# Kernel tuning notes

Measured on AMD Instinct MI355X. Metric: run time of the kernel, lower is better.

The kernel has to match this reference:

```python
import jax, jax.numpy as jnp
import numpy as np

# ---- constants from init_kwargs ----
RES = 128                       # config.grid.resolution (base_resolution, n_levels=1)
LOG2_T = 22
TABLE_SIZE = 1 << LOG2_T        # hashmap entries
N_G = 4                         # features per level, gaussian grid
N_V = 8                         # features per level, vmf grid
BB_MIN = jnp.array([-10.0, -10.0, -10.0], dtype=jnp.float32)
BB_MAX = jnp.array([10.0, 10.0, 10.0], dtype=jnp.float32)
N_PTS = 1048576

_P2 = np.uint32(2654435761)
_P3 = np.uint32(805459861)
# 8 trilinear corner offsets [8,3]
_CORNERS = jnp.array([[i, j, k] for i in (0, 1) for j in (0, 1) for k in (0, 1)], dtype=jnp.int32)


def hashgrid_lookup(table, pos):
    """tcnn-style HashGrid (1 level, trilinear). pos: [N,3] in [0,1] domain."""
    x = pos * RES                     # scale to grid coords
    x0 = jnp.floor(x)
    w = x - x0                        # [N,3] trilinear weights
    corners = x0.astype(jnp.int32)[:, None, :] + _CORNERS[None]   # [N,8,3]
    cu = corners.astype(jnp.uint32)
    h = (cu[..., 0] ^ (cu[..., 1] * _P2) ^ (cu[..., 2] * _P3)) & jnp.uint32(TABLE_SIZE - 1)
    feat = table[h.astype(jnp.int32)]                              # [N,8,F] gather
    wts = jnp.prod(jnp.where(_CORNERS[None].astype(bool), w[:, None, :], 1.0 - w[:, None, :]), axis=-1)  # [N,8]
    return jnp.einsum('nc,ncf->nf', wts, feat)                     # [N,F]


def sample_vpls(pos, gauss_table, vmf_table):
    """Accumulate encodings over the 27-neighbor stencil (accumulate_gaussians=True)."""
    block = 1.0 / RES
    npos = (pos - BB_MIN) / (BB_MAX - BB_MIN)      # normalized [N,3]
    total_g = jnp.zeros((pos.shape[0], N_G), dtype=jnp.float32)
    total_v = jnp.zeros((pos.shape[0], N_V), dtype=jnp.float32)
    for dx in (-1, 0, 1):
        for dy in (-1, 0, 1):
            for dz in (-1, 0, 1):
                off = jnp.array([dx, dy, dz], dtype=jnp.float32) * block
                p = npos + off
                total_g = total_g + hashgrid_lookup(gauss_table, p)
                total_v = total_v + hashgrid_lookup(vmf_table, p)
    return total_g, total_v


def encode(gaussians, vmf):
    # gaussian_mean_encoding='sigmoid' (non-raw -> rescale to bbox)
    mean = jax.nn.sigmoid(gaussians[:, :3]) * (BB_MAX - BB_MIN) + BB_MIN
    variance = jax.nn.softplus(gaussians[:, 3])[:, None]          # 'softplus'
    sharpness = jnp.exp(vmf[:, 0])[:, None]                        # 'exp'
    ax = vmf[:, 1:4]                                               # 'normalize' (F.normalize, eps=1e-12)
    axis = ax / jnp.maximum(jnp.linalg.norm(ax, axis=1, keepdims=True), 1e-12)
    amplitude = jax.nn.sigmoid(vmf[:, 4:7])                        # 'sigmoid'
    g_out = jnp.concatenate([mean, variance], axis=1)             # [N,4]
    v_out = jnp.concatenate([sharpness, axis, amplitude], axis=1) # [N,7]
    return g_out, v_out


def setup_inputs() -> dict:
    key = jax.random.key(0)
    k1, k2, k3 = jax.random.split(key, 3)
    # world-space query positions inside the bounding box
    u = jax.random.uniform(k1, (N_PTS, 3), dtype=jnp.float32)
    pos = u * (BB_MAX - BB_MIN) + BB_MIN
    # hash-grid feature tables (tcnn initializes near zero)
    gauss_table = jax.random.normal(k2, (TABLE_SIZE, N_G), dtype=jnp.float32) * 0.1
    vmf_table = jax.random.normal(k3, (TABLE_SIZE, N_V), dtype=jnp.float32) * 0.1
    return {"pos": pos, "gauss_table": gauss_table, "vmf_table": vmf_table}


def reference(pos, gauss_table, vmf_table):
    gaussians, vmf = sample_vpls(pos, gauss_table, vmf_table)
    return encode(gaussians, vmf)
```

## Files before the change

### kernel.cpp

```cpp
#include <hip/hip_runtime.h>
#include <hip/hip_fp16.h>
#include <cstdint>

#define TABLE_MASK 0x3FFFFFu
#define P2 2654435761u
#define P3 805459861u

#define DIM 134
#define NCELLS ((size_t)DIM * DIM * DIM)
#define RECU 8
#define NB3 (128 * 128 * 8)
#define SCAN_BLKS (NB3 / 1024)

__device__ __forceinline__ float sigmoidf_(float x) { return 1.0f / (1.0f + expf(-x)); }

__device__ __forceinline__ float2 h2f2(uint32_t u) {
    __half2 h = *reinterpret_cast<__half2*>(&u);
    return __half22float2(h);
}
__device__ __forceinline__ uint32_t f2h2(float a, float b) {
    __half2 h = __floats2half2_rn(a, b);
    return *reinterpret_cast<uint32_t*>(&h);
}

__global__ __launch_bounds__(256)
void build_dense_kernel(const float4* __restrict__ gauss,
                        const float4* __restrict__ vmf,
                        uint32_t* __restrict__ dense16)
{
    uint32_t l = blockIdx.x * blockDim.x + threadIdx.x;
    if (l >= (uint32_t)NCELLS) return;
    uint32_t cx = l % DIM;
    uint32_t t  = l / DIM;
    uint32_t cy = t % DIM;
    uint32_t cz = t / DIM;
    uint32_t ux = (uint32_t)((int)cx - 2);
    uint32_t uy = (uint32_t)((int)cy - 2);
    uint32_t uz = (uint32_t)((int)cz - 2);
    uint32_t h = (ux ^ (uy * P2) ^ (uz * P3)) & TABLE_MASK;
    float4 g  = gauss[h];
    float4 v0 = vmf[(size_t)2 * h];
    float4 v1 = vmf[(size_t)2 * h + 1];
    uint4 lo, hi;
    lo.x = f2h2(g.x,  g.y);  lo.y = f2h2(g.z,  g.w);
    lo.z = f2h2(v0.x, v0.y); lo.w = f2h2(v0.z, v0.w);
    hi.x = f2h2(v1.x, v1.y); hi.y = f2h2(v1.z, v1.w);
    hi.z = 0u; hi.w = 0u;
    uint32_t* d = dense16 + (size_t)l * RECU;
    *(uint4*)(d)     = lo;
    *(uint4*)(d + 4) = hi;
}

__device__ __forceinline__ int bin_key3(float px, float py, float pz)
{
    float x = ((px + 10.0f) / 20.0f) * 128.0f;
    float y = ((py + 10.0f) / 20.0f) * 128.0f;
    float z = ((pz + 10.0f) / 20.0f) * 128.0f;
    int ix = min(max((int)floorf(x), 0), 127);
    int iy = min(max((int)floorf(y), 0), 127);
    int iz = min(max((int)floorf(z), 0), 127);
    return (((iz << 7) + iy) << 3) + (ix >> 4);
}

__global__ __launch_bounds__(256)
void hist_kernel(const float* __restrict__ pos, uint32_t* __restrict__ hist, int n)
{
    int p = blockIdx.x * blockDim.x + threadIdx.x;
    if (p >= n) return;
    int k = bin_key3(pos[3 * p], pos[3 * p + 1], pos[3 * p + 2]);
    atomicAdd(&hist[k], 1u);
}

__global__ __launch_bounds__(1024)
void scanA_kernel(const uint32_t* __restrict__ hist,
                  uint32_t* __restrict__ cursor,
                  uint32_t* __restrict__ sums)
{
    __shared__ uint32_t buf[1024];
    int t = threadIdx.x;
    int base = blockIdx.x * 1024;
    uint32_t v = hist[base + t];
    buf[t] = v;
    __syncthreads();
    for (int off = 1; off < 1024; off <<= 1) {
        uint32_t x = (t >= off) ? buf[t - off] : 0u;
        __syncthreads();
        buf[t] += x;
        __syncthreads();
    }
    cursor[base + t] = buf[t] - v;
    if (t == 1023) sums[blockIdx.x] = buf[t];
}

__global__ __launch_bounds__(SCAN_BLKS)
void scanB_kernel(const uint32_t* __restrict__ sums, uint32_t* __restrict__ offs)
{
    __shared__ uint32_t buf[SCAN_BLKS];
    int t = threadIdx.x;
    uint32_t v = sums[t];
    buf[t] = v;
    __syncthreads();
    for (int off = 1; off < SCAN_BLKS; off <<= 1) {
        uint32_t x = (t >= off) ? buf[t - off] : 0u;
        __syncthreads();
        buf[t] += x;
        __syncthreads();
    }
    offs[t] = buf[t] - v;
}

__global__ __launch_bounds__(256)
void scatter_kernel(const float* __restrict__ pos,
                    uint32_t* __restrict__ cursor,
                    const uint32_t* __restrict__ offs,
                    float4* __restrict__ sortedPts, int n)
{
    int p = blockIdx.x * blockDim.x + threadIdx.x;
    if (p >= n) return;
    float px = pos[3 * p], py = pos[3 * p + 1], pz = pos[3 * p + 2];
    int k = bin_key3(px, py, pz);
    uint32_t slot = offs[k >> 10] + atomicAdd(&cursor[k], 1u);
    sortedPts[slot] = make_float4(px, py, pz, __uint_as_float((uint32_t)p));
}

__global__ __launch_bounds__(256, 4)
void vapl_grid_sorted_kernel(const float4* __restrict__ sortedPts,
                             const uint32_t* __restrict__ dense16,
                             float* __restrict__ out,
                             int n)
{
    int bid = blockIdx.x;
    int nb  = gridDim.x;
    int b2  = ((nb & 7) == 0) ? ((bid & 7) * (nb >> 3) + (bid >> 3)) : bid;
    int s = b2 * (int)blockDim.x + (int)threadIdx.x;
    if (s >= n) return;

    float4 pt = sortedPts[s];
    int p = (int)__float_as_uint(pt.w);

    float x = ((pt.x + 10.0f) / 20.0f) * 128.0f;
    float y = ((pt.y + 10.0f) / 20.0f) * 128.0f;
    float z = ((pt.z + 10.0f) / 20.0f) * 128.0f;

    float fx = floorf(x), fy = floorf(y), fz = floorf(z);
    int ix = (int)fx, iy = (int)fy, iz = (int)fz;
    float wx = x - fx, wy = y - fy, wz = z - fz;

    float ax[4] = {1.0f - wx, 1.0f, 1.0f, wx};
    float ay[4] = {1.0f - wy, 1.0f, 1.0f, wy};
    float az[4] = {1.0f - wz, 1.0f, 1.0f, wz};

    int bx = ix + 1, by = iy + 1, bz = iz + 1;

    float tg0 = 0.f, tg1 = 0.f, tg2 = 0.f, tg3 = 0.f;
    float tv0 = 0.f, tv1 = 0.f, tv2 = 0.f, tv3 = 0.f;
    float tv4 = 0.f, tv5 = 0.f, tv6 = 0.f, tv7 = 0.f;

    for (int k = 0; k < 4; ++k) {
        float azk = az[k];
        size_t planeBase = ((size_t)(bz + k) * DIM + (size_t)by) * DIM + (size_t)bx;
#pragma unroll
        for (int j = 0; j < 4; ++j) {
            const uint32_t* r = dense16 + (planeBase + (size_t)j * DIM) * RECU;
            float wyz = ay[j] * azk;
#pragma unroll
            for (int i = 0; i < 4; ++i) {
                uint4 A = *(const uint4*)(r + (size_t)i * RECU);
                uint2 B = *(const uint2*)(r + (size_t)i * RECU + 4);
                float w = ax[i] * wyz;
                float2 f;
                f = h2f2(A.x); tg0 = fmaf(w, f.x, tg0); tg1 = fmaf(w, f.y, tg1);
                f = h2f2(A.y); tg2 = fmaf(w, f.x, tg2); tg3 = fmaf(w, f.y, tg3);
                f = h2f2(A.z); tv0 = fmaf(w, f.x, tv0); tv1 = fmaf(w, f.y, tv1);
                f = h2f2(A.w); tv2 = fmaf(w, f.x, tv2); tv3 = fmaf(w, f.y, tv3);
                f = h2f2(B.x); tv4 = fmaf(w, f.x, tv4); tv5 = fmaf(w, f.y, tv5);
                f = h2f2(B.y); tv6 = fmaf(w, f.x, tv6); tv7 = fmaf(w, f.y, tv7);
            }
        }
    }

    float m0 = sigmoidf_(tg0) * 20.0f - 10.0f;
    float m1 = sigmoidf_(tg1) * 20.0f - 10.0f;
    float m2 = sigmoidf_(tg2) * 20.0f - 10.0f;
    float var = fmaxf(tg3, 0.0f) + log1pf(expf(-fabsf(tg3)));

    float sharp = expf(tv0);
    float nrm = fmaxf(sqrtf(tv1 * tv1 + tv2 * tv2 + tv3 * tv3), 1e-12f);
    float a0 = tv1 / nrm, a1 = tv2 / nrm, a2 = tv3 / nrm;
    float amp0 = sigmoidf_(tv4);
    float amp1 = sigmoidf_(tv5);
    float amp2 = sigmoidf_(tv6);

    float* og = out + (size_t)p * 4;
    *(float4*)og = make_float4(m0, m1, m2, var);

    float* ov = out + (size_t)n * 4 + (size_t)p * 7;
    ov[0] = sharp;
    ov[1] = a0;
    ov[2] = a1;
    ov[3] = a2;
    ov[4] = amp0;
    ov[5] = amp1;
    ov[6] = amp2;
}

__global__ __launch_bounds__(256)
void vapl_grid_kernel(const float* __restrict__ pos,
                      const float4* __restrict__ gauss,
                      const float4* __restrict__ vmf,
                      float* __restrict__ out,
                      int n)
{
    int p = blockIdx.x * blockDim.x + threadIdx.x;
    if (p >= n) return;

    float px = pos[3 * p + 0];
    float py = pos[3 * p + 1];
    float pz = pos[3 * p + 2];

    float x = ((px + 10.0f) / 20.0f) * 128.0f;
    float y = ((py + 10.0f) / 20.0f) * 128.0f;
    float z = ((pz + 10.0f) / 20.0f) * 128.0f;

    float fx = floorf(x), fy = floorf(y), fz = floorf(z);
    int ix = (int)fx, iy = (int)fy, iz = (int)fz;
    float wx = x - fx, wy = y - fy, wz = z - fz;

    float ax[4] = {1.0f - wx, 1.0f, 1.0f, wx};
    float ay[4] = {1.0f - wy, 1.0f, 1.0f, wy};
    float az[4] = {1.0f - wz, 1.0f, 1.0f, wz};

    uint32_t hx[4], hy[4], hz[4];
#pragma unroll
    for (int i = 0; i < 4; ++i) {
        hx[i] = (uint32_t)(ix - 1 + i);
        hy[i] = (uint32_t)(iy - 1 + i) * P2;
        hz[i] = (uint32_t)(iz - 1 + i) * P3;
    }

    float tg0 = 0.f, tg1 = 0.f, tg2 = 0.f, tg3 = 0.f;
    float tv0 = 0.f, tv1 = 0.f, tv2 = 0.f, tv3 = 0.f;
    float tv4 = 0.f, tv5 = 0.f, tv6 = 0.f, tv7 = 0.f;

    for (int k = 0; k < 4; ++k) {
        for (int j = 0; j < 4; ++j) {
            uint32_t hyz = hy[j] ^ hz[k];
            float wyz = ay[j] * az[k];
#pragma unroll
            for (int i = 0; i < 4; ++i) {
                uint32_t h = (hx[i] ^ hyz) & TABLE_MASK;
                float w = ax[i] * wyz;
                float4 g  = gauss[h];
                float4 v0 = vmf[(size_t)2 * h];
                float4 v1 = vmf[(size_t)2 * h + 1];
                tg0 = fmaf(w, g.x,  tg0);
                tg1 = fmaf(w, g.y,  tg1);
                tg2 = fmaf(w, g.z,  tg2);
                tg3 = fmaf(w, g.w,  tg3);
                tv0 = fmaf(w, v0.x, tv0);
                tv1 = fmaf(w, v0.y, tv1);
                tv2 = fmaf(w, v0.z, tv2);
                tv3 = fmaf(w, v0.w, tv3);
                tv4 = fmaf(w, v1.x, tv4);
                tv5 = fmaf(w, v1.y, tv5);
                tv6 = fmaf(w, v1.z, tv6);
                tv7 = fmaf(w, v1.w, tv7);
            }
        }
    }

    float m0 = sigmoidf_(tg0) * 20.0f - 10.0f;
    float m1 = sigmoidf_(tg1) * 20.0f - 10.0f;
    float m2 = sigmoidf_(tg2) * 20.0f - 10.0f;
    float var = fmaxf(tg3, 0.0f) + log1pf(expf(-fabsf(tg3)));

    float sharp = expf(tv0);
    float nrm = fmaxf(sqrtf(tv1 * tv1 + tv2 * tv2 + tv3 * tv3), 1e-12f);
    float a0 = tv1 / nrm, a1 = tv2 / nrm, a2 = tv3 / nrm;
    float amp0 = sigmoidf_(tv4);
    float amp1 = sigmoidf_(tv5);
    float amp2 = sigmoidf_(tv6);

    float* og = out + (size_t)p * 4;
    og[0] = m0;
    og[1] = m1;
    og[2] = m2;
    og[3] = var;

    float* ov = out + (size_t)n * 4 + (size_t)p * 7;
    ov[0] = sharp;
    ov[1] = a0;
    ov[2] = a1;
    ov[3] = a2;
    ov[4] = amp0;
    ov[5] = amp1;
    ov[6] = amp2;
}

extern "C" void kernel_launch(void* const* d_in, const int* in_sizes, int n_in,
                              void* d_out, int out_size, void* d_ws, size_t ws_size,
                              hipStream_t stream) {
    const float*  pos   = (const float*)d_in[0];
    const float4* gauss = (const float4*)d_in[1];
    const float4* vmf   = (const float4*)d_in[2];
    float* out = (float*)d_out;
    int n = in_sizes[0] / 3;

    size_t off = 0;
    char* ws = (char*)d_ws;
    uint32_t* dense16 = (uint32_t*)(ws + off);  off += NCELLS * RECU * 4;
    off = (off + 255) & ~(size_t)255;
    uint32_t* hist    = (uint32_t*)(ws + off);  off += (size_t)NB3 * 4;
    uint32_t* cursor  = (uint32_t*)(ws + off);  off += (size_t)NB3 * 4;
    uint32_t* sums    = (uint32_t*)(ws + off);  off += 256 * 4;
    uint32_t* offs    = (uint32_t*)(ws + off);  off += 256 * 4;
    off = (off + 255) & ~(size_t)255;
    float4* sortedPts = (float4*)(ws + off);    off += (size_t)n * 16;
    const size_t need = off;

    dim3 block(256);
    dim3 grid((n + 255) / 256);

    if (ws_size >= need) {
        dim3 bgrid((unsigned)((NCELLS + 255) / 256));
        hipLaunchKernelGGL(build_dense_kernel, bgrid, block, 0, stream, gauss, vmf, dense16);
        hipMemsetAsync(hist, 0, (size_t)NB3 * 4, stream);
        hipLaunchKernelGGL(hist_kernel, grid, block, 0, stream, pos, hist, n);
        hipLaunchKernelGGL(scanA_kernel, dim3(SCAN_BLKS), dim3(1024), 0, stream, hist, cursor, sums);
        hipLaunchKernelGGL(scanB_kernel, dim3(1), dim3(SCAN_BLKS), 0, stream, sums, offs);
        hipLaunchKernelGGL(scatter_kernel, grid, block, 0, stream, pos, cursor, offs, sortedPts, n);
        hipLaunchKernelGGL(vapl_grid_sorted_kernel, grid, block, 0, stream,
                           sortedPts, dense16, out, n);
    } else {
        hipLaunchKernelGGL(vapl_grid_kernel, grid, block, 0, stream, pos, gauss, vmf, out, n);
    }
}
```

Measured before the change: 297.4 us.

## Prefold x-axis stencil sums into dense grid to cut per-point gathers

The dense prebuilt grid now stores, per cell, the 3-cell x-direction sum and the difference of the outer cells (E and D) in fp16. That lets the sorted kernel collapse each 4-wide x row into one record, evaluated as E + wx*D, so it does 16 gathers instead of 64. The build kernel is restructured to stage two rows of table features in shared memory and compute the sums there. The main loop is also double-buffered over z-slabs, with launch bounds relaxed to 3 waves. The risk is fp16 rounding error from the hfma2 on the prefolded sums, plus a larger 48-byte record.

```diff
diff --git a/kernel.cpp b/kernel.cpp
--- a/kernel.cpp
+++ b/kernel.cpp
@@ -6,49 +6,75 @@
 #define P2 2654435761u
 #define P3 805459861u
 
-#define DIM 134
-#define NCELLS ((size_t)DIM * DIM * DIM)
-#define RECU 8
+#define XD 128
+#define YD 132
+#define ZD 132
+#define RECU 12
 #define NB3 (128 * 128 * 8)
 #define SCAN_BLKS (NB3 / 1024)
 
 __device__ __forceinline__ float sigmoidf_(float x) { return 1.0f / (1.0f + expf(-x)); }
 
-__device__ __forceinline__ float2 h2f2(uint32_t u) {
-    __half2 h = *reinterpret_cast<__half2*>(&u);
-    return __half22float2(h);
-}
 __device__ __forceinline__ uint32_t f2h2(float a, float b) {
     __half2 h = __floats2half2_rn(a, b);
     return *reinterpret_cast<uint32_t*>(&h);
 }
+__device__ __forceinline__ __half2 u2h2(uint32_t u) {
+    return *reinterpret_cast<__half2*>(&u);
+}
 
 __global__ __launch_bounds__(256)
-void build_dense_kernel(const float4* __restrict__ gauss,
-                        const float4* __restrict__ vmf,
-                        uint32_t* __restrict__ dense16)
-{
-    uint32_t l = blockIdx.x * blockDim.x + threadIdx.x;
-    if (l >= (uint32_t)NCELLS) return;
-    uint32_t cx = l % DIM;
-    uint32_t t  = l / DIM;
-    uint32_t cy = t % DIM;
-    uint32_t cz = t / DIM;
-    uint32_t ux = (uint32_t)((int)cx - 2);
-    uint32_t uy = (uint32_t)((int)cy - 2);
-    uint32_t uz = (uint32_t)((int)cz - 2);
-    uint32_t h = (ux ^ (uy * P2) ^ (uz * P3)) & TABLE_MASK;
-    float4 g  = gauss[h];
-    float4 v0 = vmf[(size_t)2 * h];
-    float4 v1 = vmf[(size_t)2 * h + 1];
-    uint4 lo, hi;
-    lo.x = f2h2(g.x,  g.y);  lo.y = f2h2(g.z,  g.w);
-    lo.z = f2h2(v0.x, v0.y); lo.w = f2h2(v0.z, v0.w);
-    hi.x = f2h2(v1.x, v1.y); hi.y = f2h2(v1.z, v1.w);
-    hi.z = 0u; hi.w = 0u;
-    uint32_t* d = dense16 + (size_t)l * RECU;
-    *(uint4*)(d)     = lo;
-    *(uint4*)(d + 4) = hi;
+void build_exdx_kernel(const float4* __restrict__ gauss,
+                       const float4* __restrict__ vmf,
+                       uint32_t* __restrict__ exdx)
+{
+    __shared__ float sm[2][131][13];
+    int bidx = blockIdx.x;
+    int yp = bidx % 66;
+    int rz = 1 + bidx / 66;
+    int ry0 = 1 + 2 * yp;
+    int t = threadIdx.x;
+
+    for (int l = t; l < 262; l += 256) {
+        int row = (l >= 131) ? 1 : 0;
+        int cell = l - row * 131;
+        int ry = ry0 + row;
+        if (ry <= 131) {
+            int xc = 1 + cell;
+            uint32_t ux = (uint32_t)(xc - 2);
+            uint32_t uy = (uint32_t)(ry - 2);
+            uint32_t uz = (uint32_t)(rz - 2);
+            uint32_t h = (ux ^ (uy * P2) ^ (uz * P3)) & TABLE_MASK;
+            float4 g  = gauss[h];
+            float4 v0 = vmf[(size_t)2 * h];
+            float4 v1 = vmf[(size_t)2 * h + 1];
+            float* s = sm[row][cell];
+            s[0] = g.x;  s[1] = g.y;  s[2]  = g.z;  s[3]  = g.w;
+            s[4] = v0.x; s[5] = v0.y; s[6]  = v0.z; s[7]  = v0.w;
+            s[8] = v1.x; s[9] = v1.y; s[10] = v1.z; s[11] = v1.w;
+        }
+    }
+    __syncthreads();
+
+    int row = t >> 7;
+    int c   = t & 127;
+    int ry  = ry0 + row;
+    if (ry > 131) return;
+
+    uint32_t rec[12];
+#pragma unroll
+    for (int m = 0; m < 6; ++m) {
+        float e0 = sm[row][c][2*m]   + sm[row][c+1][2*m]   + sm[row][c+2][2*m];
+        float e1 = sm[row][c][2*m+1] + sm[row][c+1][2*m+1] + sm[row][c+2][2*m+1];
+        float d0 = sm[row][c+3][2*m]   - sm[row][c][2*m];
+        float d1 = sm[row][c+3][2*m+1] - sm[row][c][2*m+1];
+        rec[m]     = f2h2(e0, e1);
+        rec[6 + m] = f2h2(d0, d1);
+    }
+    size_t o = (((size_t)rz * YD + (size_t)ry) * XD + (size_t)c) * RECU;
+    *(uint4*)(exdx + o)     = make_uint4(rec[0], rec[1], rec[2],  rec[3]);
+    *(uint4*)(exdx + o + 4) = make_uint4(rec[4], rec[5], rec[6],  rec[7]);
+    *(uint4*)(exdx + o + 8) = make_uint4(rec[8], rec[9], rec[10], rec[11]);
 }
 
 __device__ __forceinline__ int bin_key3(float px, float py, float pz)
@@ -123,9 +149,23 @@
     sortedPts[slot] = make_float4(px, py, pz, __uint_as_float((uint32_t)p));
 }
 
-__global__ __launch_bounds__(256, 4)
+__device__ __forceinline__ void consume_cell(const uint4& A, const uint4& B, const uint4& C,
+                                             __half2 wxh, float w, float* acc)
+{
+    uint32_t e[6] = {A.x, A.y, A.z, A.w, B.x, B.y};
+    uint32_t d[6] = {B.z, B.w, C.x, C.y, C.z, C.w};
+#pragma unroll
+    for (int m = 0; m < 6; ++m) {
+        __half2 v = __hfma2(wxh, u2h2(d[m]), u2h2(e[m]));
+        float2 f = __half22float2(v);
+        acc[2*m]     = fmaf(w, f.x, acc[2*m]);
+        acc[2*m + 1] = fmaf(w, f.y, acc[2*m + 1]);
+    }
+}
+
+__global__ __launch_bounds__(256, 3)
 void vapl_grid_sorted_kernel(const float4* __restrict__ sortedPts,
-                             const uint32_t* __restrict__ dense16,
+                             const uint32_t* __restrict__ exdx,
                              float* __restrict__ out,
                              int n)
 {
@@ -146,50 +186,64 @@
     int ix = (int)fx, iy = (int)fy, iz = (int)fz;
     float wx = x - fx, wy = y - fy, wz = z - fz;
 
-    float ax[4] = {1.0f - wx, 1.0f, 1.0f, wx};
     float ay[4] = {1.0f - wy, 1.0f, 1.0f, wy};
     float az[4] = {1.0f - wz, 1.0f, 1.0f, wz};
+    __half2 wxh = __float2half2_rn(wx);
 
     int bx = ix + 1, by = iy + 1, bz = iz + 1;
 
-    float tg0 = 0.f, tg1 = 0.f, tg2 = 0.f, tg3 = 0.f;
-    float tv0 = 0.f, tv1 = 0.f, tv2 = 0.f, tv3 = 0.f;
-    float tv4 = 0.f, tv5 = 0.f, tv6 = 0.f, tv7 = 0.f;
-
+    uint32_t idx16[16];
+    float    w16[16];
+#pragma unroll
     for (int k = 0; k < 4; ++k) {
-        float azk = az[k];
-        size_t planeBase = ((size_t)(bz + k) * DIM + (size_t)by) * DIM + (size_t)bx;
 #pragma unroll
         for (int j = 0; j < 4; ++j) {
-            const uint32_t* r = dense16 + (planeBase + (size_t)j * DIM) * RECU;
-            float wyz = ay[j] * azk;
-#pragma unroll
-            for (int i = 0; i < 4; ++i) {
-                uint4 A = *(const uint4*)(r + (size_t)i * RECU);
-                uint2 B = *(const uint2*)(r + (size_t)i * RECU + 4);
-                float w = ax[i] * wyz;
-                float2 f;
-                f = h2f2(A.x); tg0 = fmaf(w, f.x, tg0); tg1 = fmaf(w, f.y, tg1);
-                f = h2f2(A.y); tg2 = fmaf(w, f.x, tg2); tg3 = fmaf(w, f.y, tg3);
-                f = h2f2(A.z); tv0 = fmaf(w, f.x, tv0); tv1 = fmaf(w, f.y, tv1);
-                f = h2f2(A.w); tv2 = fmaf(w, f.x, tv2); tv3 = fmaf(w, f.y, tv3);
-                f = h2f2(B.x); tv4 = fmaf(w, f.x, tv4); tv5 = fmaf(w, f.y, tv5);
-                f = h2f2(B.y); tv6 = fmaf(w, f.x, tv6); tv7 = fmaf(w, f.y, tv7);
+            idx16[k*4 + j] = (((uint32_t)(bz + k) * YD + (uint32_t)(by + j)) * XD
+                              + (uint32_t)(bx - 1)) * RECU;
+            w16[k*4 + j] = ay[j] * az[k];
+        }
+    }
+
+    float acc[12] = {0.f,0.f,0.f,0.f,0.f,0.f,0.f,0.f,0.f,0.f,0.f,0.f};
+
+    uint4 buf[2][4][3];
+#pragma unroll
+    for (int c = 0; c < 4; ++c) {
+        const uint32_t* r = exdx + idx16[c];
+        buf[0][c][0] = *(const uint4*)(r);
+        buf[0][c][1] = *(const uint4*)(r + 4);
+        buf[0][c][2] = *(const uint4*)(r + 8);
+    }
+#pragma unroll
+    for (int b = 0; b < 4; ++b) {
+        const int cur = b & 1, nxt = cur ^ 1;
+        if (b < 3) {
+#pragma unroll
+            for (int c = 0; c < 4; ++c) {
+                const uint32_t* r = exdx + idx16[(b + 1) * 4 + c];
+                buf[nxt][c][0] = *(const uint4*)(r);
+                buf[nxt][c][1] = *(const uint4*)(r + 4);
+                buf[nxt][c][2] = *(const uint4*)(r + 8);
             }
         }
-    }
-
-    float m0 = sigmoidf_(tg0) * 20.0f - 10.0f;
-    float m1 = sigmoidf_(tg1) * 20.0f - 10.0f;
-    float m2 = sigmoidf_(tg2) * 20.0f - 10.0f;
-    float var = fmaxf(tg3, 0.0f) + log1pf(expf(-fabsf(tg3)));
-
-    float sharp = expf(tv0);
-    float nrm = fmaxf(sqrtf(tv1 * tv1 + tv2 * tv2 + tv3 * tv3), 1e-12f);
-    float a0 = tv1 / nrm, a1 = tv2 / nrm, a2 = tv3 / nrm;
-    float amp0 = sigmoidf_(tv4);
-    float amp1 = sigmoidf_(tv5);
-    float amp2 = sigmoidf_(tv6);
+#pragma unroll
+        for (int c = 0; c < 4; ++c) {
+            consume_cell(buf[cur][c][0], buf[cur][c][1], buf[cur][c][2],
+                         wxh, w16[b*4 + c], acc);
+        }
+    }
+
+    float m0 = sigmoidf_(acc[0]) * 20.0f - 10.0f;
+    float m1 = sigmoidf_(acc[1]) * 20.0f - 10.0f;
+    float m2 = sigmoidf_(acc[2]) * 20.0f - 10.0f;
+    float var = fmaxf(acc[3], 0.0f) + log1pf(expf(-fabsf(acc[3])));
+
+    float sharp = expf(acc[4]);
+    float nrm = fmaxf(sqrtf(acc[5]*acc[5] + acc[6]*acc[6] + acc[7]*acc[7]), 1e-12f);
+    float a0 = acc[5] / nrm, a1 = acc[6] / nrm, a2 = acc[7] / nrm;
+    float amp0 = sigmoidf_(acc[8]);
+    float amp1 = sigmoidf_(acc[9]);
+    float amp2 = sigmoidf_(acc[10]);
 
     float* og = out + (size_t)p * 4;
     *(float4*)og = make_float4(m0, m1, m2, var);
@@ -308,29 +362,29 @@
 
     size_t off = 0;
     char* ws = (char*)d_ws;
-    uint32_t* dense16 = (uint32_t*)(ws + off);  off += NCELLS * RECU * 4;
+    uint32_t* exdx   = (uint32_t*)(ws + off);  off += (size_t)XD * YD * ZD * RECU * 4;
     off = (off + 255) & ~(size_t)255;
-    uint32_t* hist    = (uint32_t*)(ws + off);  off += (size_t)NB3 * 4;
-    uint32_t* cursor  = (uint32_t*)(ws + off);  off += (size_t)NB3 * 4;
-    uint32_t* sums    = (uint32_t*)(ws + off);  off += 256 * 4;
-    uint32_t* offs    = (uint32_t*)(ws + off);  off += 256 * 4;
+    uint32_t* hist   = (uint32_t*)(ws + off);  off += (size_t)NB3 * 4;
+    uint32_t* cursor = (uint32_t*)(ws + off);  off += (size_t)NB3 * 4;
+    uint32_t* sums   = (uint32_t*)(ws + off);  off += 256 * 4;
+    uint32_t* offs   = (uint32_t*)(ws + off);  off += 256 * 4;
     off = (off + 255) & ~(size_t)255;
-    float4* sortedPts = (float4*)(ws + off);    off += (size_t)n * 16;
+    float4* sortedPts = (float4*)(ws + off);   off += (size_t)n * 16;
     const size_t need = off;
 
     dim3 block(256);
     dim3 grid((n + 255) / 256);
 
     if (ws_size >= need) {
-        dim3 bgrid((unsigned)((NCELLS + 255) / 256));
-        hipLaunchKernelGGL(build_dense_kernel, bgrid, block, 0, stream, gauss, vmf, dense16);
+        dim3 bgrid(131 * 66);
+        hipLaunchKernelGGL(build_exdx_kernel, bgrid, block, 0, stream, gauss, vmf, exdx);
         hipMemsetAsync(hist, 0, (size_t)NB3 * 4, stream);
         hipLaunchKernelGGL(hist_kernel, grid, block, 0, stream, pos, hist, n);
         hipLaunchKernelGGL(scanA_kernel, dim3(SCAN_BLKS), dim3(1024), 0, stream, hist, cursor, sums);
         hipLaunchKernelGGL(scanB_kernel, dim3(1), dim3(SCAN_BLKS), 0, stream, sums, offs);
         hipLaunchKernelGGL(scatter_kernel, grid, block, 0, stream, pos, cursor, offs, sortedPts, n);
         hipLaunchKernelGGL(vapl_grid_sorted_kernel, grid, block, 0, stream,
-                           sortedPts, dense16, out, n);
+                           sortedPts, exdx, out, n);
     } else {
         hipLaunchKernelGGL(vapl_grid_kernel, grid, block, 0, stream, pos, gauss, vmf, out, n);
     }
```

After: 267.1 us. 10.2% less time.
